# Kernel tuning notes

Measured on AMD Instinct MI355X. Metric: run time of the kernel, lower is better.

The kernel has to match this reference:

```python
import jax, jax.numpy as jnp
import numpy as np

L, B, N, D = 8, 2, 512, 1024      # ensemble size, batch, seq, model dim
H, DH = 8, 64                      # heads, dim_head
INNER = H * DH
M = 2 * L                          # messages = [tokens, ensemble_out] concatenated on dim 0
SCALE = DH ** -0.5


def rmsnorm(x, w, eps):
    return x * jax.lax.rsqrt(jnp.mean(x * x, axis=-1, keepdims=True) + eps) * w


def setup_inputs() -> dict:
    key = jax.random.key(0)
    ks = jax.random.split(key, 8)
    bound = D ** -0.5
    tokens = jax.random.normal(ks[0], (L, B, N, D), dtype=jnp.float32)
    # per-member Linear(dim, dim): torch weight [out,in] -> stored [L, D, D]
    w_net = jax.random.uniform(ks[1], (L, D, D), jnp.float32, -bound, bound)
    b_net = jnp.zeros((L, D), jnp.float32)
    # voting attention params (stored transposed so x @ W works)
    norm_w = jnp.ones((D,), jnp.float32)
    knorm_w = jnp.ones((DH,), jnp.float32)
    wq = jax.random.uniform(ks[2], (D, INNER), jnp.float32, -bound, bound)
    wkv = jax.random.uniform(ks[3], (D, 2 * INNER), jnp.float32, -bound, bound)
    wg = jax.random.uniform(ks[4], (D, H), jnp.float32, -bound, bound)
    wout = jax.random.uniform(ks[5], (INNER, D), jnp.float32, -(INNER ** -0.5), INNER ** -0.5)
    return dict(tokens=tokens, w_net=w_net, b_net=b_net, norm_w=norm_w,
                wq=wq, wkv=wkv, knorm_w=knorm_w, wg=wg, wout=wout)


def reference(tokens, w_net, b_net, norm_w, wq, wkv, knorm_w, wg, wout):
    eps = jnp.finfo(tokens.dtype).eps
    # vmapped sub-network: per-member Linear
    out = jnp.einsum('lbnd,lod->lbno', tokens, w_net) + b_net[:, None, None, :]
    # messages = cat([tokens, out], dim=0) -> context of M=2L messages per (b,n)
    ctx = jnp.concatenate([tokens, out], axis=0)            # [M,B,N,D]
    # voting attention: queries are the tokens (len-1 per position), kv over M messages.
    # original tiles ctx over l ('m b ... d -> (lq b) ... m d'); we broadcast instead.
    tn = rmsnorm(tokens, norm_w, eps)                        # query norm only
    q = (tn @ wq).reshape(L, B, N, H, DH)
    kv = ctx @ wkv                                           # [M,B,N,2*INNER]
    k, v = jnp.split(kv, 2, axis=-1)
    k = rmsnorm(k.reshape(M, B, N, H, DH), knorm_w, eps)
    v = v.reshape(M, B, N, H, DH)
    sim = jnp.einsum('lbnhd,mbnhd->lbnhm', q, k) * SCALE
    attn = jax.nn.softmax(sim, axis=-1)
    o = jnp.einsum('lbnhm,mbnhd->lbnhd', attn, v)
    gates = jax.nn.sigmoid(tn @ wg)                          # [L,B,N,H]
    o = o * gates[..., None]
    pooled = o.reshape(L, B, N, INNER) @ wout                # [L,B,N,D]
    return pooled
```

## Files before the change

kernel.cpp:

```cpp
#include <hip/hip_runtime.h>
#include <hip/hip_bf16.h>
#include <math.h>

#define L_ 8
#define B_ 2
#define N_ 512
#define D_ 1024
#define H_ 8
#define DH_ 64
#define INNER_ 512
#define M_ 16
#define BN_TOK 1024
#define EPS 1.1920928955078125e-07f
#define SCALE_ 0.125f

typedef __attribute__((ext_vector_type(8))) __bf16 bf16x8;
typedef __attribute__((ext_vector_type(4))) __bf16 bf16x4;
typedef __attribute__((ext_vector_type(4))) float f32x4;

#define BARF() do { __builtin_amdgcn_s_barrier(); __builtin_amdgcn_sched_barrier(0); } while (0)
#define GLL(SRC, DST) __builtin_amdgcn_global_load_lds( \
    (const __attribute__((address_space(1))) void*)(SRC), \
    (__attribute__((address_space(3))) void*)(DST), 16, 0, 0)

__global__ __launch_bounds__(256) void rs_kernel(
    const float* __restrict__ tokens, const float* __restrict__ norm_w,
    __bf16* __restrict__ tok_bf, __bf16* __restrict__ tn_bf)
{
    const int row = blockIdx.x;
    const int t = threadIdx.x;
    const int wave = t >> 6, lane = t & 63;
    __shared__ float wsum[4];

    const float4 v = ((const float4*)(tokens + (size_t)row * D_))[t];
    float ss = fmaf(v.x, v.x, fmaf(v.y, v.y, fmaf(v.z, v.z, v.w * v.w)));
    #pragma unroll
    for (int o = 1; o < 64; o <<= 1) ss += __shfl_xor(ss, o);
    if (lane == 0) wsum[wave] = ss;
    __syncthreads();
    const float rsv = rsqrtf((wsum[0] + wsum[1] + wsum[2] + wsum[3]) * (1.f / D_) + EPS);

    const float4 nw = ((const float4*)norm_w)[t];
    bf16x4 tb; tb.x = (__bf16)v.x; tb.y = (__bf16)v.y; tb.z = (__bf16)v.z; tb.w = (__bf16)v.w;
    ((bf16x4*)(tok_bf + (size_t)row * D_))[t] = tb;
    bf16x4 nb;
    nb.x = (__bf16)(v.x * rsv * nw.x); nb.y = (__bf16)(v.y * rsv * nw.y);
    nb.z = (__bf16)(v.z * rsv * nw.z); nb.w = (__bf16)(v.w * rsv * nw.w);
    ((bf16x4*)(tn_bf + (size_t)row * D_))[t] = nb;
}

__global__ __launch_bounds__(256) void wgT_kernel(
    const float* __restrict__ wg, __bf16* __restrict__ wgT)
{
    const int g = blockIdx.x * 256 + threadIdx.x;
    const int h = g >> 10, d = g & 1023;
    wgT[g] = (h < 8) ? (__bf16)wg[d * 8 + h] : (__bf16)0.f;
}

__global__ __launch_bounds__(256) void gates_kernel(
    const __bf16* __restrict__ tn, const __bf16* __restrict__ wgT,
    float* __restrict__ gates_out)
{
    const int w = threadIdx.x >> 6, lane = threadIdx.x & 63;
    const int fr = lane & 15, fq = lane >> 4;
    const int r0 = blockIdx.x * 64 + w * 16;
    const __bf16* arow = tn + (size_t)(r0 + fr) * D_ + fq * 8;
    const __bf16* brow = wgT + (size_t)fr * D_ + fq * 8;
    f32x4 acc = (f32x4){0.f, 0.f, 0.f, 0.f};
    #pragma unroll 8
    for (int k0 = 0; k0 < D_; k0 += 32) {
        bf16x8 a = *(const bf16x8*)(arow + k0);
        bf16x8 b = *(const bf16x8*)(brow + k0);
        acc = __builtin_amdgcn_mfma_f32_16x16x32_bf16(a, b, acc, 0, 0, 0);
    }
    if (fr < 8) {
        #pragma unroll
        for (int r = 0; r < 4; ++r)
            gates_out[(size_t)(r0 + fq * 4 + r) * H_ + fr] = 1.f / (1.f + expf(-acc[r]));
    }
}

__global__ __launch_bounds__(256) void convert_bf16_kernel(
    const float* __restrict__ in, __bf16* __restrict__ out)
{
    const int i = blockIdx.x * 256 + threadIdx.x;
    float4 v = ((const float4*)in)[i];
    bf16x4 o;
    o.x = (__bf16)v.x; o.y = (__bf16)v.y; o.z = (__bf16)v.z; o.w = (__bf16)v.w;
    *(bf16x4*)(out + (size_t)i * 4) = o;
}

__global__ __launch_bounds__(256) void transpose_convert_kernel(
    const float* __restrict__ in, __bf16* __restrict__ out, int R, int C)
{
    __shared__ float tile[32][33];
    const int bx = blockIdx.x;
    const int by = blockIdx.y;
    const int x = threadIdx.x & 31, y = threadIdx.x >> 5;
    #pragma unroll
    for (int r = 0; r < 4; ++r)
        tile[y + r * 8][x] = in[(size_t)(by * 32 + y + r * 8) * C + bx * 32 + x];
    __syncthreads();
    #pragma unroll
    for (int r = 0; r < 4; ++r)
        out[(size_t)(bx * 32 + y + r * 8) * R + by * 32 + x] = (__bf16)tile[x][y + r * 8];
}

template <int MODE>
__global__ __launch_bounds__(512, 2) void gemm_big(
    const __bf16* __restrict__ A, const __bf16* __restrict__ A2,
    const __bf16* __restrict__ Bt, const __bf16* __restrict__ Bt2,
    const float* __restrict__ bias,
    void* __restrict__ Cout, void* __restrict__ Cout2)
{
    __shared__ __align__(16) __bf16 As[2][256 * 64];
    __shared__ __align__(16) __bf16 Bs[2][256 * 64];

    constexpr int NT = (MODE == 0) ? 8 : 16;
    constexpr int K = NT * 64;

    const int tid = threadIdx.x;
    const int w = tid >> 6, lane = tid & 63;
    const int wm = w >> 2, wn = w & 3;
    const int fr = lane & 15, fq = lane >> 4;

    const int bid = blockIdx.x;
    int m0, n0, Ncols;
    const __bf16 *Ab, *Btb;
    const float* biasp = nullptr;
    void* Co;

    if (MODE == 4) {
        const bool isq = bid >= 128;
        const int b2 = isq ? bid - 128 : bid;
        const int ntx = isq ? 2 : 4;
        const int c = b2 & 7, s = b2 >> 3;
        const int sq = s / ntx;
        m0 = (c * 4 + sq) * 256;
        n0 = (s - sq * ntx) * 256;
        if (isq) {
            Ab = A2 + (size_t)m0 * K; Btb = Bt2 + (size_t)n0 * K;
            Co = Cout2; Ncols = 512;
        } else {
            Ab = A + (size_t)m0 * K;
            Btb = Bt + (size_t)(m0 >> 10) * 1024 * K + (size_t)n0 * K;
            Co = Cout; Ncols = 1024;
            biasp = bias + (size_t)(m0 >> 10) * 1024;
        }
    } else {
        const int ntx = 4;
        const int nty8 = (MODE == 3) ? 8 : 4;
        const int c = bid & 7, s = bid >> 3;
        const int sq = s / ntx;
        m0 = (c * nty8 + sq) * 256;
        n0 = (s - sq * ntx) * 256;
        Ncols = 1024;
        Co = Cout;
        if (MODE == 3)
            Ab = (m0 >= 8192) ? (A2 + (size_t)(m0 - 8192) * K) : (A + (size_t)m0 * K);
        else
            Ab = A + (size_t)m0 * K;
        Btb = Bt + (size_t)n0 * K;
    }

    const int lrow = lane >> 3;
    const int lchunk = (lane & 7) ^ lrow;
    const int fo0 = ((fq ^ (lane & 7)) << 4);
    const int fo1 = (((4 + fq) ^ (lane & 7)) << 4);

#define STAGE_A(T2, PB, HALF) do {                                            \
    _Pragma("unroll")                                                         \
    for (int ld = (HALF) * 2; ld < (HALF) * 2 + 2; ++ld)                      \
        GLL(Ab + (size_t)(w * 32 + ld * 8 + lrow) * K + (T2) * 64 + lchunk * 8, \
            &As[PB][(w * 32 + ld * 8) * 64]);                                 \
} while (0)
#define STAGE_B(T2, PB, HALF) do {                                            \
    _Pragma("unroll")                                                         \
    for (int ld = (HALF) * 2; ld < (HALF) * 2 + 2; ++ld)                      \
        GLL(Btb + (size_t)(w * 32 + ld * 8 + lrow) * K + (T2) * 64 + lchunk * 8, \
            &Bs[PB][(w * 32 + ld * 8) * 64]);                                 \
} while (0)
#define READ_FRAGS(AFR, BFR, FO) do {                                         \
    _Pragma("unroll")                                                         \
    for (int mi = 0; mi < 8; ++mi)                                            \
        (AFR)[mi] = *(const bf16x8*)(Ap + ((wm * 128 + mi * 16 + fr) << 7) + (FO)); \
    _Pragma("unroll")                                                         \
    for (int nj = 0; nj < 4; ++nj)                                            \
        (BFR)[nj] = *(const bf16x8*)(Bp + ((wn * 64 + nj * 16 + fr) << 7) + (FO)); \
} while (0)
#define MFMA16(AOFF, AFR, BFR) do {                                           \
    _Pragma("unroll")                                                         \
    for (int mi = 0; mi < 4; ++mi)                                            \
        _Pragma("unroll")                                                     \
        for (int nj = 0; nj < 4; ++nj)                                        \
            acc[(AOFF) + mi][nj] = __builtin_amdgcn_mfma_f32_16x16x32_bf16(   \
                (AFR)[(AOFF) + mi], (BFR)[nj], acc[(AOFF) + mi][nj], 0, 0, 0); \
} while (0)

    f32x4 acc[8][4];
    #pragma unroll
    for (int mi = 0; mi < 8; ++mi)
        #pragma unroll
        for (int nj = 0; nj < 4; ++nj)
            acc[mi][nj] = (f32x4){0.f, 0.f, 0.f, 0.f};

    STAGE_A(0, 0, 0); STAGE_A(0, 0, 1);
    STAGE_B(0, 0, 0); STAGE_B(0, 0, 1);
    STAGE_A(1, 1, 0); STAGE_A(1, 1, 1);
    asm volatile("s_waitcnt vmcnt(4)" ::: "memory");
    BARF();

    for (int t = 0; t < NT; ++t) {
        const int p = t & 1;
        const char* Ap = (const char*)&As[p][0];
        const char* Bp = (const char*)&Bs[p][0];
        bf16x8 af0[8], af1[8], bf0[4], bf1[4];

        READ_FRAGS(af0, bf0, fo0);
        if (t + 1 < NT) STAGE_B(t + 1, p ^ 1, 0);
        BARF();
        __builtin_amdgcn_s_setprio(1);
        MFMA16(0, af0, bf0);
        __builtin_amdgcn_s_setprio(0);
        BARF();

        READ_FRAGS(af1, bf1, fo1);
        if (t + 1 < NT) STAGE_B(t + 1, p ^ 1, 1);
        BARF();
        __builtin_amdgcn_s_setprio(1);
        MFMA16(4, af0, bf0);
        __builtin_amdgcn_s_setprio(0);
        asm volatile("s_waitcnt lgkmcnt(0)" ::: "memory");
        BARF();

        if (t + 2 < NT) STAGE_A(t + 2, p, 0);
        BARF();
        __builtin_amdgcn_s_setprio(1);
        MFMA16(0, af1, bf1);
        __builtin_amdgcn_s_setprio(0);
        BARF();

        if (t + 2 < NT) STAGE_A(t + 2, p, 1);
        BARF();
        __builtin_amdgcn_s_setprio(1);
        MFMA16(4, af1, bf1);
        __builtin_amdgcn_s_setprio(0);
        if (t + 2 < NT) { asm volatile("s_waitcnt vmcnt(4)" ::: "memory"); }
        else            { asm volatile("s_waitcnt vmcnt(0)" ::: "memory"); }
        BARF();
    }

    #pragma unroll
    for (int mi = 0; mi < 8; ++mi) {
        const int r0 = m0 + wm * 128 + mi * 16 + fq * 4;
        #pragma unroll
        for (int nj = 0; nj < 4; ++nj) {
            const int col = n0 + wn * 64 + nj * 16 + fr;
            const float badd = (MODE == 4 && biasp != nullptr) ? biasp[col] : 0.f;
            #pragma unroll
            for (int r = 0; r < 4; ++r) {
                float v = acc[mi][nj][r] + badd;
                if (MODE == 0)
                    ((float*)Co)[(size_t)(r0 + r) * Ncols + col] = v;
                else
                    ((__bf16*)Co)[(size_t)(r0 + r) * Ncols + col] = (__bf16)v;
            }
        }
    }
#undef STAGE_A
#undef STAGE_B
#undef READ_FRAGS
#undef MFMA16
}

__global__ __launch_bounds__(64) void attn_kernel(
    const __bf16* __restrict__ q,
    const __bf16* __restrict__ kv,
    const float* __restrict__ gates,
    const float* __restrict__ knw,
    __bf16* __restrict__ og)
{
    const int bid = blockIdx.x;
    const int c = bid & 7;
    const int s = bid >> 3;
    const int bn = c * 128 + (s >> 3);
    const int h = s & 7;
    const int t = threadIdx.x;

    __shared__ __align__(16) float qs[8][65];
    __shared__ __align__(16) float ks[16][65];
    __shared__ __align__(16) float vs[16][65];
    __shared__ float ss[8][17];
    __shared__ float kscale[16];
    __shared__ float gs[8];

    const float kw = knw[t];
    #pragma unroll
    for (int l = 0; l < 8; ++l)
        qs[l][t] = (float)q[((size_t)(l * BN_TOK + bn)) * INNER_ + h * DH_ + t] * kw;
    #pragma unroll
    for (int m = 0; m < 16; ++m) {
        const __bf16* kvrow = kv + ((size_t)(m * BN_TOK + bn)) * (2 * INNER_) + h * DH_;
        ks[m][t] = (float)kvrow[t];
        vs[m][t] = (float)kvrow[INNER_ + t];
    }
    if (t < 8) gs[t] = gates[((size_t)(t * BN_TOK + bn)) * H_ + h];
    __syncthreads();

    {
        int m = t & 15, grp = t >> 4;
        float s2 = 0.f;
        #pragma unroll
        for (int j = 0; j < 16; ++j) { float v = ks[m][grp * 16 + j]; s2 = fmaf(v, v, s2); }
        s2 += __shfl_xor(s2, 16);
        s2 += __shfl_xor(s2, 32);
        if (grp == 0) kscale[m] = rsqrtf(s2 * (1.f / DH_) + EPS);
    }
    __syncthreads();

    #pragma unroll
    for (int r = 0; r < 2; ++r) {
        int p = t + r * 64;
        int l = p >> 4, m = p & 15;
        float s2 = 0.f;
        #pragma unroll
        for (int d = 0; d < 64; ++d) s2 = fmaf(qs[l][d], ks[m][d], s2);
        ss[l][m] = s2 * kscale[m] * SCALE_;
    }
    __syncthreads();

    if (t < 8) {
        float mx = -1e30f;
        #pragma unroll
        for (int m = 0; m < 16; ++m) mx = fmaxf(mx, ss[t][m]);
        float sum = 0.f;
        #pragma unroll
        for (int m = 0; m < 16; ++m) { float e = expf(ss[t][m] - mx); ss[t][m] = e; sum += e; }
        float inv = 1.f / sum;
        #pragma unroll
        for (int m = 0; m < 16; ++m) ss[t][m] *= inv;
    }
    __syncthreads();

    #pragma unroll
    for (int l = 0; l < 8; ++l) {
        float o = 0.f;
        #pragma unroll
        for (int m = 0; m < 16; ++m) o = fmaf(ss[l][m], vs[m][t], o);
        og[((size_t)(l * BN_TOK + bn)) * INNER_ + h * DH_ + t] = (__bf16)(o * gs[l]);
    }
}

extern "C" void kernel_launch(void* const* d_in, const int* in_sizes, int n_in,
                              void* d_out, int out_size, void* d_ws, size_t ws_size,
                              hipStream_t stream)
{
    const float* tokens = (const float*)d_in[0];
    const float* w_net  = (const float*)d_in[1];
    const float* b_net  = (const float*)d_in[2];
    const float* norm_w = (const float*)d_in[3];
    const float* wq     = (const float*)d_in[4];
    const float* wkv    = (const float*)d_in[5];
    const float* knw    = (const float*)d_in[6];
    const float* wg     = (const float*)d_in[7];
    const float* wout   = (const float*)d_in[8];
    float* out = (float*)d_out;

    char* ws = (char*)d_ws;
    __bf16* tok_bf  = (__bf16*)(ws);
    __bf16* tn_bf   = (__bf16*)(ws + 16777216);
    __bf16* out_bf  = (__bf16*)(ws + 33554432);
    __bf16* q_bf    = (__bf16*)(ws + 50331648);
    __bf16* kv_bf   = (__bf16*)(ws + 58720256);
    __bf16* og_bf   = (__bf16*)(ws + 92274688);
    __bf16* wnet_bf = (__bf16*)(ws + 100663296);
    __bf16* wqt_bf  = (__bf16*)(ws + 117440512);
    __bf16* wkvt_bf = (__bf16*)(ws + 118489088);
    __bf16* woutt_bf= (__bf16*)(ws + 120586240);
    float*  ws_g    = (float*)(ws + 121667584);
    __bf16* wgT_bf  = (__bf16*)(ws + 121929728);

    rs_kernel<<<L_ * BN_TOK, 256, 0, stream>>>(tokens, norm_w, tok_bf, tn_bf);
    convert_bf16_kernel<<<8192, 256, 0, stream>>>(w_net, wnet_bf);
    transpose_convert_kernel<<<dim3(16, 32), 256, 0, stream>>>(wq, wqt_bf, 1024, 512);
    transpose_convert_kernel<<<dim3(32, 32), 256, 0, stream>>>(wkv, wkvt_bf, 1024, 1024);
    transpose_convert_kernel<<<dim3(32, 16), 256, 0, stream>>>(wout, woutt_bf, 512, 1024);
    wgT_kernel<<<64, 256, 0, stream>>>(wg, wgT_bf);

    gates_kernel<<<128, 256, 0, stream>>>(tn_bf, wgT_bf, ws_g);

    gemm_big<4><<<192, 512, 0, stream>>>(tok_bf, tn_bf, wnet_bf, wqt_bf, b_net,
                                         (void*)out_bf, (void*)q_bf);
    gemm_big<3><<<256, 512, 0, stream>>>(tok_bf, out_bf, wkvt_bf, nullptr, nullptr,
                                         (void*)kv_bf, nullptr);
    attn_kernel<<<BN_TOK * H_, 64, 0, stream>>>(q_bf, kv_bf, ws_g, knw, og_bf);
    gemm_big<0><<<128, 512, 0, stream>>>(og_bf, nullptr, woutt_bf, nullptr, nullptr,
                                         (void*)out, nullptr);
}
```

Baseline: 155.1 us.

## Finer-grained GEMM fragment pipelining and per-token attention blocks with vector loads

```diff
diff --git a/kernel.cpp b/kernel.cpp
--- a/kernel.cpp
+++ b/kernel.cpp
@@ -180,21 +180,23 @@
         GLL(Btb + (size_t)(w * 32 + ld * 8 + lrow) * K + (T2) * 64 + lchunk * 8, \
             &Bs[PB][(w * 32 + ld * 8) * 64]);                                 \
 } while (0)
-#define READ_FRAGS(AFR, BFR, FO) do {                                         \
+#define RD_A(DST, MIOFF, FO) do {                                             \
     _Pragma("unroll")                                                         \
-    for (int mi = 0; mi < 8; ++mi)                                            \
-        (AFR)[mi] = *(const bf16x8*)(Ap + ((wm * 128 + mi * 16 + fr) << 7) + (FO)); \
+    for (int mi = 0; mi < 4; ++mi)                                            \
+        (DST)[mi] = *(const bf16x8*)(Ap + ((wm * 128 + ((MIOFF) + mi) * 16 + fr) << 7) + (FO)); \
+} while (0)
+#define RD_B(DST, FO) do {                                                    \
     _Pragma("unroll")                                                         \
     for (int nj = 0; nj < 4; ++nj)                                            \
-        (BFR)[nj] = *(const bf16x8*)(Bp + ((wn * 64 + nj * 16 + fr) << 7) + (FO)); \
+        (DST)[nj] = *(const bf16x8*)(Bp + ((wn * 64 + nj * 16 + fr) << 7) + (FO)); \
 } while (0)
-#define MFMA16(AOFF, AFR, BFR) do {                                           \
+#define MFMA4(AFR, BFR, AOFF) do {                                            \
     _Pragma("unroll")                                                         \
     for (int mi = 0; mi < 4; ++mi)                                            \
         _Pragma("unroll")                                                     \
         for (int nj = 0; nj < 4; ++nj)                                        \
             acc[(AOFF) + mi][nj] = __builtin_amdgcn_mfma_f32_16x16x32_bf16(   \
-                (AFR)[(AOFF) + mi], (BFR)[nj], acc[(AOFF) + mi][nj], 0, 0, 0); \
+                (AFR)[mi], (BFR)[nj], acc[(AOFF) + mi][nj], 0, 0, 0);         \
 } while (0)
 
     f32x4 acc[8][4];
@@ -214,36 +216,35 @@
         const int p = t & 1;
         const char* Ap = (const char*)&As[p][0];
         const char* Bp = (const char*)&Bs[p][0];
-        bf16x8 af0[8], af1[8], bf0[4], bf1[4];
-
-        READ_FRAGS(af0, bf0, fo0);
+        bf16x8 a0[4], a1[4], a2[4], a3[4], b0[4], b1[4];
+
+        RD_A(a0, 0, fo0); RD_B(b0, fo0);
         if (t + 1 < NT) STAGE_B(t + 1, p ^ 1, 0);
         BARF();
+
+        RD_A(a1, 4, fo0);
+        if (t + 1 < NT) STAGE_B(t + 1, p ^ 1, 1);
         __builtin_amdgcn_s_setprio(1);
-        MFMA16(0, af0, bf0);
+        MFMA4(a0, b0, 0);
         __builtin_amdgcn_s_setprio(0);
         BARF();
 
-        READ_FRAGS(af1, bf1, fo1);
-        if (t + 1 < NT) STAGE_B(t + 1, p ^ 1, 1);
-        BARF();
+        RD_A(a2, 0, fo1); RD_B(b1, fo1); RD_A(a3, 4, fo1);
         __builtin_amdgcn_s_setprio(1);
-        MFMA16(4, af0, bf0);
+        MFMA4(a1, b0, 4);
         __builtin_amdgcn_s_setprio(0);
         asm volatile("s_waitcnt lgkmcnt(0)" ::: "memory");
         BARF();
 
         if (t + 2 < NT) STAGE_A(t + 2, p, 0);
-        BARF();
         __builtin_amdgcn_s_setprio(1);
-        MFMA16(0, af1, bf1);
+        MFMA4(a2, b1, 0);
         __builtin_amdgcn_s_setprio(0);
         BARF();
 
         if (t + 2 < NT) STAGE_A(t + 2, p, 1);
-        BARF();
         __builtin_amdgcn_s_setprio(1);
-        MFMA16(4, af1, bf1);
+        MFMA4(a3, b1, 4);
         __builtin_amdgcn_s_setprio(0);
         if (t + 2 < NT) { asm volatile("s_waitcnt vmcnt(4)" ::: "memory"); }
         else            { asm volatile("s_waitcnt vmcnt(0)" ::: "memory"); }
@@ -269,85 +270,95 @@
     }
 #undef STAGE_A
 #undef STAGE_B
-#undef READ_FRAGS
-#undef MFMA16
-}
-
-__global__ __launch_bounds__(64) void attn_kernel(
+#undef RD_A
+#undef RD_B
+#undef MFMA4
+}
+
+__global__ __launch_bounds__(512) void attn_kernel(
     const __bf16* __restrict__ q,
     const __bf16* __restrict__ kv,
     const float* __restrict__ gates,
     const float* __restrict__ knw,
     __bf16* __restrict__ og)
 {
-    const int bid = blockIdx.x;
-    const int c = bid & 7;
-    const int s = bid >> 3;
-    const int bn = c * 128 + (s >> 3);
-    const int h = s & 7;
-    const int t = threadIdx.x;
-
-    __shared__ __align__(16) float qs[8][65];
-    __shared__ __align__(16) float ks[16][65];
-    __shared__ __align__(16) float vs[16][65];
-    __shared__ float ss[8][17];
-    __shared__ float kscale[16];
-    __shared__ float gs[8];
-
-    const float kw = knw[t];
-    #pragma unroll
-    for (int l = 0; l < 8; ++l)
-        qs[l][t] = (float)q[((size_t)(l * BN_TOK + bn)) * INNER_ + h * DH_ + t] * kw;
-    #pragma unroll
-    for (int m = 0; m < 16; ++m) {
-        const __bf16* kvrow = kv + ((size_t)(m * BN_TOK + bn)) * (2 * INNER_) + h * DH_;
-        ks[m][t] = (float)kvrow[t];
-        vs[m][t] = (float)kvrow[INNER_ + t];
-    }
-    if (t < 8) gs[t] = gates[((size_t)(t * BN_TOK + bn)) * H_ + h];
+    const int bn = blockIdx.x;
+    const int tid = threadIdx.x;
+    const int h = tid >> 6, lane = tid & 63;
+
+    __shared__ __align__(16) __bf16 qs[8][520];
+    __shared__ __align__(16) __bf16 kvs[16][1032];
+    __shared__ float ssm[8][8][17];
+    __shared__ float kn[64];
+    __shared__ float gs[64];
+
+    {
+        const int l = tid >> 6, c8 = tid & 63;
+        *(bf16x8*)&qs[l][c8 * 8] =
+            *(const bf16x8*)(q + ((size_t)(l * BN_TOK + bn)) * INNER_ + c8 * 8);
+    }
+    #pragma unroll
+    for (int i = 0; i < 4; ++i) {
+        const int g = tid + i * 512;
+        const int m = g >> 7, c8 = g & 127;
+        *(bf16x8*)&kvs[m][c8 * 8] =
+            *(const bf16x8*)(kv + ((size_t)(m * BN_TOK + bn)) * 1024 + c8 * 8);
+    }
+    if (tid < 64) {
+        kn[tid] = knw[tid];
+        gs[tid] = gates[((size_t)((tid >> 3) * BN_TOK + bn)) * H_ + (tid & 7)];
+    }
     __syncthreads();
 
-    {
-        int m = t & 15, grp = t >> 4;
-        float s2 = 0.f;
-        #pragma unroll
-        for (int j = 0; j < 16; ++j) { float v = ks[m][grp * 16 + j]; s2 = fmaf(v, v, s2); }
-        s2 += __shfl_xor(s2, 16);
-        s2 += __shfl_xor(s2, 32);
-        if (grp == 0) kscale[m] = rsqrtf(s2 * (1.f / DH_) + EPS);
-    }
-    __syncthreads();
-
-    #pragma unroll
-    for (int r = 0; r < 2; ++r) {
-        int p = t + r * 64;
-        int l = p >> 4, m = p & 15;
-        float s2 = 0.f;
-        #pragma unroll
-        for (int d = 0; d < 64; ++d) s2 = fmaf(qs[l][d], ks[m][d], s2);
-        ss[l][m] = s2 * kscale[m] * SCALE_;
-    }
-    __syncthreads();
-
-    if (t < 8) {
-        float mx = -1e30f;
-        #pragma unroll
-        for (int m = 0; m < 16; ++m) mx = fmaxf(mx, ss[t][m]);
-        float sum = 0.f;
-        #pragma unroll
-        for (int m = 0; m < 16; ++m) { float e = expf(ss[t][m] - mx); ss[t][m] = e; sum += e; }
-        float inv = 1.f / sum;
-        #pragma unroll
-        for (int m = 0; m < 16; ++m) ss[t][m] *= inv;
-    }
-    __syncthreads();
-
+    const int m = lane & 15, grp = lane >> 4;
+
+    float s2 = 0.f;
+    #pragma unroll
+    for (int j = 0; j < 16; ++j) {
+        float v = (float)kvs[m][h * DH_ + grp * 16 + j];
+        s2 = fmaf(v, v, s2);
+    }
+    s2 += __shfl_xor(s2, 16);
+    s2 += __shfl_xor(s2, 32);
+    const float kscale = rsqrtf(s2 * (1.f / DH_) + EPS) * SCALE_;
+
+    const int l0 = grp, l1 = grp + 4;
+    float sim0 = 0.f, sim1 = 0.f;
+    #pragma unroll
+    for (int d = 0; d < DH_; ++d) {
+        const float kf = (float)kvs[m][h * DH_ + d] * kn[d];
+        sim0 = fmaf((float)qs[l0][h * DH_ + d], kf, sim0);
+        sim1 = fmaf((float)qs[l1][h * DH_ + d], kf, sim1);
+    }
+    sim0 *= kscale; sim1 *= kscale;
+
+    float mx0 = sim0, mx1 = sim1;
+    #pragma unroll
+    for (int o = 1; o < 16; o <<= 1) {
+        mx0 = fmaxf(mx0, __shfl_xor(mx0, o));
+        mx1 = fmaxf(mx1, __shfl_xor(mx1, o));
+    }
+    float e0 = expf(sim0 - mx0), e1 = expf(sim1 - mx1);
+    float sm0 = e0, sm1 = e1;
+    #pragma unroll
+    for (int o = 1; o < 16; o <<= 1) {
+        sm0 += __shfl_xor(sm0, o);
+        sm1 += __shfl_xor(sm1, o);
+    }
+    ssm[h][l0][m] = e0 / sm0;
+    ssm[h][l1][m] = e1 / sm1;
+
+    float vf[16];
+    #pragma unroll
+    for (int mm = 0; mm < 16; ++mm)
+        vf[mm] = (float)kvs[mm][INNER_ + h * DH_ + lane];
     #pragma unroll
     for (int l = 0; l < 8; ++l) {
         float o = 0.f;
         #pragma unroll
-        for (int m = 0; m < 16; ++m) o = fmaf(ss[l][m], vs[m][t], o);
-        og[((size_t)(l * BN_TOK + bn)) * INNER_ + h * DH_ + t] = (__bf16)(o * gs[l]);
+        for (int mm = 0; mm < 16; ++mm) o = fmaf(ssm[h][l][mm], vf[mm], o);
+        og[((size_t)(l * BN_TOK + bn)) * INNER_ + h * DH_ + lane] =
+            (__bf16)(o * gs[l * 8 + h]);
     }
 }
 
@@ -393,7 +404,7 @@
                                          (void*)out_bf, (void*)q_bf);
     gemm_big<3><<<256, 512, 0, stream>>>(tok_bf, out_bf, wkvt_bf, nullptr, nullptr,
                                          (void*)kv_bf, nullptr);
-    attn_kernel<<<BN_TOK * H_, 64, 0, stream>>>(q_bf, kv_bf, ws_g, knw, og_bf);
+    attn_kernel<<<BN_TOK, 512, 0, stream>>>(q_bf, kv_bf, ws_g, knw, og_bf);
     gemm_big<0><<<128, 512, 0, stream>>>(og_bf, nullptr, woutt_bf, nullptr, nullptr,
                                          (void*)out, nullptr);
 }
```

After: 150.1 us. 1.03x faster.
